# Kernel optimization log

Measured on AMD Instinct MI355X. Metric: run time of the kernel, lower is better.

The kernel has to match this reference:

```python
import jax, jax.numpy as jnp
import numpy as np

N_NODES = 50000
N_EDGES = 300000
F_IN, HID, N_CLS = 256, 256, 128


def _glorot_linear(key, fan_in, fan_out):
    # torch.nn.Linear-style uniform init, kaiming bound 1/sqrt(fan_in)
    s = 1.0 / np.sqrt(fan_in)
    return jax.random.uniform(key, (fan_in, fan_out), jnp.float32, -s, s)


def setup_inputs() -> dict:
    key = jax.random.key(0)
    ks = jax.random.split(key, 8)
    x = jax.random.normal(ks[0], (N_NODES, F_IN), jnp.float32)
    edge_index = jax.random.randint(ks[1], (2, N_EDGES), 0, N_NODES, dtype=jnp.int32)
    return {
        "x": x,
        "edge_index": edge_index,
        "W1": _glorot_linear(ks[2], F_IN, HID), "b1": jnp.zeros((HID,), jnp.float32),
        "W2": _glorot_linear(ks[3], HID, HID),  "b2": jnp.zeros((HID,), jnp.float32),
        "W3": _glorot_linear(ks[4], HID, HID),  "b3": jnp.zeros((HID,), jnp.float32),
        "W4": _glorot_linear(ks[5], HID, N_CLS), "b4": jnp.zeros((N_CLS,), jnp.float32),
    }


def _gcn_conv(x, W, b, src, dst, norm, n):
    # x' = D^{-1/2} (A + I) D^{-1/2} X W + b   (PyG GCNConv default)
    h = x @ W                                  # [N, out]
    msg = h[src] * norm[:, None]               # gather + edge scaling  [E', out]
    return jax.ops.segment_sum(msg, dst, num_segments=n) + b


def reference(x, edge_index, W1, b1, W2, b2, W3, b3, W4, b4):
    n = x.shape[0]
    loops = jnp.arange(n, dtype=edge_index.dtype)
    src = jnp.concatenate([edge_index[0], loops])  # add self-loops
    dst = jnp.concatenate([edge_index[1], loops])
    # symmetric normalization: deg over target nodes (unit edge weights)
    deg = jax.ops.segment_sum(jnp.ones_like(dst, jnp.float32), dst, num_segments=n)
    dis = jnp.where(deg > 0, jax.lax.rsqrt(jnp.maximum(deg, 1.0)), 0.0)
    norm = dis[src] * dis[dst]                     # [E']

    h = jax.nn.relu(_gcn_conv(x, W1, b1, src, dst, norm, n))
    h = jax.nn.relu(_gcn_conv(h, W2, b2, src, dst, norm, n))
    h = jax.nn.relu(_gcn_conv(h, W3, b3, src, dst, norm, n))
    h = _gcn_conv(h, W4, b4, src, dst, norm, n)    # [N, C]

    # global_add_pool with batch == zeros -> single-graph sum pool
    pooled = jnp.sum(h, axis=0, keepdims=True)     # [1, C]
    return (pooled, jax.nn.log_softmax(pooled, axis=1))
```

## Files before the change

kernel.cpp:

```cpp
#include <hip/hip_runtime.h>


typedef __attribute__((ext_vector_type(8))) short short8;
typedef __attribute__((ext_vector_type(8))) signed char schar8;
typedef __attribute__((ext_vector_type(4))) float float4v;

__device__ __forceinline__ unsigned short f2b(float f) {
    unsigned int u = __builtin_bit_cast(unsigned int, f);
    u += 0x7fffu + ((u >> 16) & 1u);
    return (unsigned short)(u >> 16);
}
__device__ __forceinline__ float b2f(unsigned short b) {
    unsigned int u = ((unsigned int)b) << 16;
    return __builtin_bit_cast(float, u);
}

__global__ void zero_convert_kernel(int* __restrict__ cnt, float* __restrict__ tsum,
                                    float* __restrict__ accbuf,
                                    const float* __restrict__ W1, const float* __restrict__ W2,
                                    const float* __restrict__ W3, unsigned short* __restrict__ Wt1,
                                    unsigned short* __restrict__ Wt2, unsigned short* __restrict__ Wt3,
                                    int N, int nb) {
    int t = threadIdx.x;
    int b = blockIdx.x;
    if (b < nb) {
        int i = b * 256 + t;
        if (i < N) { cnt[i] = 0; tsum[i] = 0.f; }
        if (b == 0) accbuf[t] = 0.f;
    } else {
        int bb = b - nb;
        int w = bb >> 8;
        int n = bb & 255;
        const float* W = (w == 0) ? W1 : (w == 1) ? W2 : W3;
        unsigned short* Wt = (w == 0) ? Wt1 : (w == 1) ? Wt2 : Wt3;
        Wt[n * 256 + t] = f2b(W[t * 256 + n]);
    }
}

__global__ void count_kernel(const int* __restrict__ dst, int* __restrict__ cnt, int E) {
    int i = blockIdx.x * blockDim.x + threadIdx.x;
    if (i < E) atomicAdd(&cnt[dst[i]], 1);
}

__global__ void blocksum_kernel(const int* __restrict__ cnt, int* __restrict__ bsum, int N) {
    __shared__ int s[256];
    int t = threadIdx.x;
    int i = blockIdx.x * 256 + t;
    s[t] = (i < N) ? cnt[i] : 0;
    __syncthreads();
    for (int d = 128; d > 0; d >>= 1) {
        if (t < d) s[t] += s[t + d];
        __syncthreads();
    }
    if (t == 0) bsum[blockIdx.x] = s[0];
}

__global__ void finalize_kernel(const int* __restrict__ cnt, const int* __restrict__ bsum,
                                int* __restrict__ offs, int* __restrict__ cursor,
                                float* __restrict__ dis, int N, int E, int nb) {
    __shared__ int bs[256];
    __shared__ int s[256];
    int t = threadIdx.x;
    bs[t] = (t < nb) ? bsum[t] : 0;
    __syncthreads();
    for (int d = 1; d < 256; d <<= 1) {
        int x = (t >= d) ? bs[t - d] : 0;
        __syncthreads();
        bs[t] += x;
        __syncthreads();
    }
    int blockoff = (blockIdx.x == 0) ? 0 : bs[blockIdx.x - 1];
    int i = blockIdx.x * 256 + t;
    int c = (i < N) ? cnt[i] : 0;
    s[t] = c;
    __syncthreads();
    for (int d = 1; d < 256; d <<= 1) {
        int x = (t >= d) ? s[t - d] : 0;
        __syncthreads();
        s[t] += x;
        __syncthreads();
    }
    if (i < N) {
        int ex = blockoff + s[t] - c;
        offs[i] = ex;
        cursor[i] = ex;
        dis[i] = rsqrtf((float)(c + 1));
    }
    if (blockIdx.x == 0 && t == 0) offs[N] = E;
}

__global__ void scatter_outsum_kernel(const int* __restrict__ src, const int* __restrict__ dst,
                                      const float* __restrict__ dis, int* __restrict__ cursor,
                                      int* __restrict__ csr_src, float* __restrict__ csr_nrm,
                                      float* __restrict__ tsum, int E) {
    int i = blockIdx.x * blockDim.x + threadIdx.x;
    if (i < E) {
        int s = src[i], d = dst[i];
        float dd = dis[d];
        int pos = atomicAdd(&cursor[d], 1);
        csr_src[pos] = s;
        csr_nrm[pos] = dis[s] * dd;
        atomicAdd(&tsum[s], dd);
    }
}

template <int AFP32>
__global__ __launch_bounds__(256, 3) void gemm_bf16_kernel(
        const void* __restrict__ Ap, const unsigned short* __restrict__ Wt,
        signed char* __restrict__ C8, float* __restrict__ Ts, int M) {
    __shared__ unsigned short As[128 * 64];
    __shared__ unsigned short Bs[128 * 64];
    const int tid = threadIdx.x;
    const int lane = tid & 63;
    const int wave = tid >> 6;
    const int l15 = lane & 15;
    const int quad = lane >> 4;
    const int wm = wave & 1;
    const int wn = wave >> 1;
    const int m0 = blockIdx.x * 128;
    const int n0 = blockIdx.y * 128;

    float4v acc[4][4] = {};

    const int lrow = lane >> 3;
    const int lslot = (lane & 7) ^ lrow;

    const unsigned short* Bt = Wt + (size_t)n0 * 256;

    for (int kk = 0; kk < 256; kk += 64) {
        if (AFP32) {
            const float* Af = (const float*)Ap;
            const int srow = tid >> 3;
            const int slot = tid & 7;
#pragma unroll
            for (int p = 0; p < 4; p++) {
                int row = p * 32 + srow;
                int gm = m0 + row;
                float4 lo = make_float4(0.f, 0.f, 0.f, 0.f);
                float4 hi = make_float4(0.f, 0.f, 0.f, 0.f);
                if (gm < M) {
                    const float* ap = &Af[(size_t)gm * 256 + kk + slot * 8];
                    lo = *(const float4*)ap;
                    hi = *(const float4*)(ap + 4);
                }
                union { unsigned short u[8]; float4 v; } pk;
                pk.u[0] = f2b(lo.x); pk.u[1] = f2b(lo.y);
                pk.u[2] = f2b(lo.z); pk.u[3] = f2b(lo.w);
                pk.u[4] = f2b(hi.x); pk.u[5] = f2b(hi.y);
                pk.u[6] = f2b(hi.z); pk.u[7] = f2b(hi.w);
                *(float4*)&As[row * 64 + 8 * (slot ^ (row & 7))] = pk.v;
            }
        } else {
            const unsigned short* Ab = (const unsigned short*)Ap;
#pragma unroll
            for (int i = 0; i < 4; i++) {
                int r0 = wave * 32 + i * 8;
                int gm = m0 + r0 + lrow;
                if (gm >= M) gm = M - 1;
                const unsigned short* gp = &Ab[(size_t)gm * 256 + kk + lslot * 8];
                __builtin_amdgcn_global_load_lds(
                    (const __attribute__((address_space(1))) unsigned int*)gp,
                    (__attribute__((address_space(3))) unsigned int*)&As[r0 * 64],
                    16, 0, 0);
            }
        }
#pragma unroll
        for (int i = 0; i < 4; i++) {
            int r0 = wave * 32 + i * 8;
            const unsigned short* gp = &Bt[(size_t)(r0 + lrow) * 256 + kk + lslot * 8];
            __builtin_amdgcn_global_load_lds(
                (const __attribute__((address_space(1))) unsigned int*)gp,
                (__attribute__((address_space(3))) unsigned int*)&Bs[r0 * 64],
                16, 0, 0);
        }
        __syncthreads();
#pragma unroll
        for (int ks = 0; ks < 64; ks += 32) {
            const int sl = (ks >> 3) + quad;
            short8 af[4], bf[4];
#pragma unroll
            for (int mi = 0; mi < 4; mi++) {
                int row = wm * 64 + mi * 16 + l15;
                af[mi] = *(const short8*)&As[row * 64 + 8 * (sl ^ (row & 7))];
            }
#pragma unroll
            for (int nj = 0; nj < 4; nj++) {
                int row = wn * 64 + nj * 16 + l15;
                bf[nj] = *(const short8*)&Bs[row * 64 + 8 * (sl ^ (row & 7))];
            }
#pragma unroll
            for (int mi = 0; mi < 4; mi++)
#pragma unroll
                for (int nj = 0; nj < 4; nj++)
                    acc[mi][nj] = __builtin_amdgcn_mfma_f32_16x16x32_bf16(
                        af[mi], bf[nj], acc[mi][nj], 0, 0, 0);
        }
        __syncthreads();
    }

    float* pmax = (float*)As;
    float* pinv = (float*)Bs;
#pragma unroll
    for (int mi = 0; mi < 4; mi++) {
#pragma unroll
        for (int r = 0; r < 4; r++) {
            float m = fabsf(acc[mi][0][r]);
            m = fmaxf(m, fabsf(acc[mi][1][r]));
            m = fmaxf(m, fabsf(acc[mi][2][r]));
            m = fmaxf(m, fabsf(acc[mi][3][r]));
            m = fmaxf(m, __shfl_xor(m, 1));
            m = fmaxf(m, __shfl_xor(m, 2));
            m = fmaxf(m, __shfl_xor(m, 4));
            m = fmaxf(m, __shfl_xor(m, 8));
            if (l15 == 0) pmax[(wm * 64 + mi * 16 + quad * 4 + r) * 2 + wn] = m;
        }
    }
    __syncthreads();
    if (tid < 128) {
        float m = fmaxf(pmax[tid * 2], pmax[tid * 2 + 1]);
        int grow = m0 + tid;
        if (grow < M) Ts[(size_t)grow * 2 + blockIdx.y] = m * (1.f / 127.f);
        pinv[tid] = (m > 0.f) ? 127.f / m : 0.f;
    }
    __syncthreads();
#pragma unroll
    for (int mi = 0; mi < 4; mi++) {
#pragma unroll
        for (int r = 0; r < 4; r++) {
            int lr = wm * 64 + mi * 16 + quad * 4 + r;
            float inv = pinv[lr];
            int row = m0 + lr;
            if (row < M) {
#pragma unroll
                for (int nj = 0; nj < 4; nj++) {
                    int col = n0 + wn * 64 + nj * 16 + l15;
                    C8[(size_t)row * 256 + col] =
                        (signed char)__float2int_rn(acc[mi][nj][r] * inv);
                }
            }
        }
    }
}

template <int RELU>
__global__ __launch_bounds__(256) void agg_bf16_kernel(
        const signed char* __restrict__ T8, const float* __restrict__ Ts,
        const float* __restrict__ bias,
        const int* __restrict__ offs, const int* __restrict__ csr_src,
        const float* __restrict__ csr_nrm, const float* __restrict__ dis,
        unsigned short* __restrict__ out, int N) {
    int hw = threadIdx.x >> 5;
    int l = threadIdx.x & 31;
    int v = blockIdx.x * 8 + hw;
    if (v >= N) return;
    int f8 = l * 8;
    int hh = l >> 4;
    int beg = offs[v], end = offs[v + 1];
    float dv = dis[v];
    float w = dv * dv * Ts[(size_t)v * 2 + hh];
    float a[8];
    {
        schar8 q = *(const schar8*)&T8[(size_t)v * 256 + f8];
#pragma unroll
        for (int i = 0; i < 8; i++) a[i] = w * (float)q[i];
    }
    int e = beg;
    for (; e + 4 <= end; e += 4) {
        int s0 = csr_src[e],     s1 = csr_src[e + 1];
        int s2 = csr_src[e + 2], s3 = csr_src[e + 3];
        float n0 = csr_nrm[e]     * Ts[(size_t)s0 * 2 + hh];
        float n1 = csr_nrm[e + 1] * Ts[(size_t)s1 * 2 + hh];
        float n2 = csr_nrm[e + 2] * Ts[(size_t)s2 * 2 + hh];
        float n3 = csr_nrm[e + 3] * Ts[(size_t)s3 * 2 + hh];
        schar8 h0 = *(const schar8*)&T8[(size_t)s0 * 256 + f8];
        schar8 h1 = *(const schar8*)&T8[(size_t)s1 * 256 + f8];
        schar8 h2 = *(const schar8*)&T8[(size_t)s2 * 256 + f8];
        schar8 h3 = *(const schar8*)&T8[(size_t)s3 * 256 + f8];
#pragma unroll
        for (int i = 0; i < 8; i++)
            a[i] += n0 * (float)h0[i] + n1 * (float)h1[i]
                  + n2 * (float)h2[i] + n3 * (float)h3[i];
    }
    for (; e < end; e++) {
        int s = csr_src[e];
        float nm = csr_nrm[e] * Ts[(size_t)s * 2 + hh];
        schar8 h = *(const schar8*)&T8[(size_t)s * 256 + f8];
#pragma unroll
        for (int i = 0; i < 8; i++) a[i] += nm * (float)h[i];
    }
    float4 bv0 = *(const float4*)&bias[f8];
    float4 bv1 = *(const float4*)&bias[f8 + 4];
    a[0] += bv0.x; a[1] += bv0.y; a[2] += bv0.z; a[3] += bv0.w;
    a[4] += bv1.x; a[5] += bv1.y; a[6] += bv1.z; a[7] += bv1.w;
    if (RELU) {
#pragma unroll
        for (int i = 0; i < 8; i++) a[i] = fmaxf(a[i], 0.f);
    }
    uint4 o;
    o.x = (unsigned int)f2b(a[0]) | ((unsigned int)f2b(a[1]) << 16);
    o.y = (unsigned int)f2b(a[2]) | ((unsigned int)f2b(a[3]) << 16);
    o.z = (unsigned int)f2b(a[4]) | ((unsigned int)f2b(a[5]) << 16);
    o.w = (unsigned int)f2b(a[6]) | ((unsigned int)f2b(a[7]) << 16);
    *(uint4*)&out[(size_t)v * 256 + f8] = o;
}

__global__ __launch_bounds__(256) void wpool_partial(
        const unsigned short* __restrict__ H, const float* __restrict__ dis,
        const float* __restrict__ tsum, float* __restrict__ partial, int N) {
    int tid = threadIdx.x;
    int f8 = (tid & 31) * 8;
    int rg = tid >> 5;
    float a[8] = {};
    for (int r = blockIdx.x * 8 + rg; r < N; r += gridDim.x * 8) {
        float s = dis[r] * (dis[r] + tsum[r]);
        short8 h = *(const short8*)&H[(size_t)r * 256 + f8];
#pragma unroll
        for (int i = 0; i < 8; i++) a[i] += s * b2f((unsigned short)h[i]);
    }
    __shared__ float red[8 * 256];
#pragma unroll
    for (int i = 0; i < 8; i++) red[rg * 256 + f8 + i] = a[i];
    __syncthreads();
    for (int s = 4; s > 0; s >>= 1) {
        if (rg < s) {
#pragma unroll
            for (int i = 0; i < 8; i++)
                red[rg * 256 + f8 + i] += red[(rg + s) * 256 + f8 + i];
        }
        __syncthreads();
    }
    partial[(size_t)blockIdx.x * 256 + tid] = red[tid];
}

__global__ void wpool_reduce(const float* __restrict__ partial, float* __restrict__ acc) {
    int f = threadIdx.x;
    int p0 = blockIdx.x * 32;
    float a = 0.f;
#pragma unroll
    for (int p = 0; p < 32; p++) a += partial[(size_t)(p0 + p) * 256 + f];
    atomicAdd(&acc[f], a);
}

__global__ void final_kernel(const float* __restrict__ acc, const float* __restrict__ W4,
                             const float* __restrict__ b4, float* __restrict__ out, int N) {
    __shared__ float red[128];
    int c = threadIdx.x;
    float p = (float)N * b4[c];
    for (int k = 0; k < 256; k++) p += acc[k] * W4[k * 128 + c];
    out[c] = p;
    red[c] = p;
    __syncthreads();
    for (int s = 64; s > 0; s >>= 1) {
        if (c < s) red[c] = fmaxf(red[c], red[c + s]);
        __syncthreads();
    }
    float m = red[0];
    __syncthreads();
    red[c] = expf(p - m);
    __syncthreads();
    for (int s = 64; s > 0; s >>= 1) {
        if (c < s) red[c] += red[c + s];
        __syncthreads();
    }
    float lse = m + logf(red[0]);
    out[128 + c] = p - lse;
}

extern "C" void kernel_launch(void* const* d_in, const int* in_sizes, int n_in,
                              void* d_out, int out_size, void* d_ws, size_t ws_size,
                              hipStream_t stream) {
    const float* x  = (const float*)d_in[0];
    const int*   ei = (const int*)d_in[1];
    const float* W1 = (const float*)d_in[2];
    const float* b1 = (const float*)d_in[3];
    const float* W2 = (const float*)d_in[4];
    const float* b2 = (const float*)d_in[5];
    const float* W3 = (const float*)d_in[6];
    const float* b3 = (const float*)d_in[7];
    const float* W4 = (const float*)d_in[8];
    const float* b4 = (const float*)d_in[9];

    const int N = in_sizes[0] / 256;
    const int E = in_sizes[1] / 2;
    const int* src = ei;
    const int* dst = ei + E;

    char* p = (char*)d_ws;
    auto alloc = [&](size_t bytes) {
        char* r = p;
        p += (bytes + 255) & ~(size_t)255;
        return r;
    };
    int*            cnt     = (int*)alloc((size_t)N * 4);
    int*            offs    = (int*)alloc((size_t)(N + 1) * 4);
    int*            cursor  = (int*)alloc((size_t)N * 4);
    float*          dis     = (float*)alloc((size_t)N * 4);
    float*          tsum    = (float*)alloc((size_t)N * 4);
    int*            bsum    = (int*)alloc(1024 * 4);
    int*            csr_src = (int*)alloc((size_t)E * 4);
    float*          csr_nrm = (float*)alloc((size_t)E * 4);
    unsigned short* Wt1     = (unsigned short*)alloc(256 * 256 * 2);
    unsigned short* Wt2     = (unsigned short*)alloc(256 * 256 * 2);
    unsigned short* Wt3     = (unsigned short*)alloc(256 * 256 * 2);
    signed char*    T8      = (signed char*)alloc((size_t)N * 256);
    float*          Ts      = (float*)alloc((size_t)N * 2 * 4);
    unsigned short* Abuf    = (unsigned short*)alloc((size_t)N * 256 * 2);
    float*          partial = (float*)alloc((size_t)1024 * 256 * 4);
    float*          accbuf  = (float*)alloc(256 * 4);

    int eb = (E + 255) / 256;
    int nb = (N + 255) / 256;
    zero_convert_kernel<<<nb + 768, 256, 0, stream>>>(cnt, tsum, accbuf,
                                                      W1, W2, W3, Wt1, Wt2, Wt3, N, nb);
    count_kernel<<<eb, 256, 0, stream>>>(dst, cnt, E);
    blocksum_kernel<<<nb, 256, 0, stream>>>(cnt, bsum, N);
    finalize_kernel<<<nb, 256, 0, stream>>>(cnt, bsum, offs, cursor, dis, N, E, nb);
    scatter_outsum_kernel<<<eb, 256, 0, stream>>>(src, dst, dis, cursor, csr_src,
                                                  csr_nrm, tsum, E);

    dim3 ggrid((N + 127) / 128, 2);
    int ab = (N + 7) / 8;
    gemm_bf16_kernel<1><<<ggrid, 256, 0, stream>>>(x, Wt1, T8, Ts, N);
    agg_bf16_kernel<1><<<ab, 256, 0, stream>>>(T8, Ts, b1, offs, csr_src, csr_nrm, dis, Abuf, N);
    gemm_bf16_kernel<0><<<ggrid, 256, 0, stream>>>(Abuf, Wt2, T8, Ts, N);
    agg_bf16_kernel<1><<<ab, 256, 0, stream>>>(T8, Ts, b2, offs, csr_src, csr_nrm, dis, Abuf, N);
    gemm_bf16_kernel<0><<<ggrid, 256, 0, stream>>>(Abuf, Wt3, T8, Ts, N);
    agg_bf16_kernel<1><<<ab, 256, 0, stream>>>(T8, Ts, b3, offs, csr_src, csr_nrm, dis, Abuf, N);

    wpool_partial<<<1024, 256, 0, stream>>>(Abuf, dis, tsum, partial, N);
    wpool_reduce<<<32, 256, 0, stream>>>(partial, accbuf);
    final_kernel<<<1, 128, 0, stream>>>(accbuf, W4, b4, (float*)d_out, N);
}
```

Measured before the change: 314.1 us.

## Double-buffer GEMM LDS tiles, pre-convert x to bf16, and swizzle block order

The GEMM now uses two LDS buffers so the async global-to-LDS load of the next K slice overlaps the MFMA work on the current one. The fp32 input x is converted to bf16 once inside the setup kernel, so the first GEMM can use the same direct-to-LDS load path as the later layers. A 1D grid with grouped block ordering puts both N-halves of neighbouring M tiles close together for better L2 reuse of A rows. In exchange, LDS use doubles and occupancy drops to 2 blocks per CU, and an extra 25MB bf16 copy of x is written and read.

```diff
diff --git a/kernel.cpp b/kernel.cpp
--- a/kernel.cpp
+++ b/kernel.cpp
@@ -20,6 +20,7 @@
                                     const float* __restrict__ W1, const float* __restrict__ W2,
                                     const float* __restrict__ W3, unsigned short* __restrict__ Wt1,
                                     unsigned short* __restrict__ Wt2, unsigned short* __restrict__ Wt3,
+                                    const float* __restrict__ x, unsigned short* __restrict__ xb,
                                     int N, int nb) {
     int t = threadIdx.x;
     int b = blockIdx.x;
@@ -27,13 +28,25 @@
         int i = b * 256 + t;
         if (i < N) { cnt[i] = 0; tsum[i] = 0.f; }
         if (b == 0) accbuf[t] = 0.f;
-    } else {
+    } else if (b < nb + 768) {
         int bb = b - nb;
         int w = bb >> 8;
         int n = bb & 255;
         const float* W = (w == 0) ? W1 : (w == 1) ? W2 : W3;
         unsigned short* Wt = (w == 0) ? Wt1 : (w == 1) ? Wt2 : Wt3;
         Wt[n * 256 + t] = f2b(W[t * 256 + n]);
+    } else {
+        size_t base = ((size_t)(b - nb - 768) * 256 + t) * 8;
+        if (base < (size_t)N * 256) {
+            float4 lo = *(const float4*)&x[base];
+            float4 hi = *(const float4*)&x[base + 4];
+            uint4 o;
+            o.x = (unsigned int)f2b(lo.x) | ((unsigned int)f2b(lo.y) << 16);
+            o.y = (unsigned int)f2b(lo.z) | ((unsigned int)f2b(lo.w) << 16);
+            o.z = (unsigned int)f2b(hi.x) | ((unsigned int)f2b(hi.y) << 16);
+            o.w = (unsigned int)f2b(hi.z) | ((unsigned int)f2b(hi.w) << 16);
+            *(uint4*)&xb[base] = o;
+        }
     }
 }
 
@@ -104,12 +117,11 @@
     }
 }
 
-template <int AFP32>
-__global__ __launch_bounds__(256, 3) void gemm_bf16_kernel(
-        const void* __restrict__ Ap, const unsigned short* __restrict__ Wt,
+__global__ __launch_bounds__(256, 2) void gemm_bf16_kernel(
+        const unsigned short* __restrict__ Ab, const unsigned short* __restrict__ Wt,
         signed char* __restrict__ C8, float* __restrict__ Ts, int M) {
-    __shared__ unsigned short As[128 * 64];
-    __shared__ unsigned short Bs[128 * 64];
+    __shared__ unsigned short As[2 * 128 * 64];
+    __shared__ unsigned short Bs[2 * 128 * 64];
     const int tid = threadIdx.x;
     const int lane = tid & 63;
     const int wave = tid >> 6;
@@ -117,8 +129,15 @@
     const int quad = lane >> 4;
     const int wm = wave & 1;
     const int wn = wave >> 1;
-    const int m0 = blockIdx.x * 128;
-    const int n0 = blockIdx.y * 128;
+
+    const int bid = blockIdx.x;
+    const int grp = bid >> 4;
+    const int ii = bid & 15;
+    const int xv = grp * 8 + (ii & 7);
+    const int yv = ii >> 3;
+    const int m0 = xv * 128;
+    const int n0 = yv * 128;
+    if (m0 >= M) return;
 
     float4v acc[4][4] = {};
 
@@ -127,53 +146,37 @@
 
     const unsigned short* Bt = Wt + (size_t)n0 * 256;
 
-    for (int kk = 0; kk < 256; kk += 64) {
-        if (AFP32) {
-            const float* Af = (const float*)Ap;
-            const int srow = tid >> 3;
-            const int slot = tid & 7;
-#pragma unroll
-            for (int p = 0; p < 4; p++) {
-                int row = p * 32 + srow;
-                int gm = m0 + row;
-                float4 lo = make_float4(0.f, 0.f, 0.f, 0.f);
-                float4 hi = make_float4(0.f, 0.f, 0.f, 0.f);
-                if (gm < M) {
-                    const float* ap = &Af[(size_t)gm * 256 + kk + slot * 8];
-                    lo = *(const float4*)ap;
-                    hi = *(const float4*)(ap + 4);
-                }
-                union { unsigned short u[8]; float4 v; } pk;
-                pk.u[0] = f2b(lo.x); pk.u[1] = f2b(lo.y);
-                pk.u[2] = f2b(lo.z); pk.u[3] = f2b(lo.w);
-                pk.u[4] = f2b(hi.x); pk.u[5] = f2b(hi.y);
-                pk.u[6] = f2b(hi.z); pk.u[7] = f2b(hi.w);
-                *(float4*)&As[row * 64 + 8 * (slot ^ (row & 7))] = pk.v;
-            }
-        } else {
-            const unsigned short* Ab = (const unsigned short*)Ap;
-#pragma unroll
-            for (int i = 0; i < 4; i++) {
-                int r0 = wave * 32 + i * 8;
-                int gm = m0 + r0 + lrow;
-                if (gm >= M) gm = M - 1;
-                const unsigned short* gp = &Ab[(size_t)gm * 256 + kk + lslot * 8];
-                __builtin_amdgcn_global_load_lds(
-                    (const __attribute__((address_space(1))) unsigned int*)gp,
-                    (__attribute__((address_space(3))) unsigned int*)&As[r0 * 64],
-                    16, 0, 0);
-            }
-        }
-#pragma unroll
-        for (int i = 0; i < 4; i++) {
-            int r0 = wave * 32 + i * 8;
-            const unsigned short* gp = &Bt[(size_t)(r0 + lrow) * 256 + kk + lslot * 8];
-            __builtin_amdgcn_global_load_lds(
-                (const __attribute__((address_space(1))) unsigned int*)gp,
-                (__attribute__((address_space(3))) unsigned int*)&Bs[r0 * 64],
-                16, 0, 0);
-        }
-        __syncthreads();
+#define GSTAGE(bufofs, kk)                                                          \
+    {                                                                               \
+        _Pragma("unroll") for (int i_ = 0; i_ < 4; i_++) {                          \
+            int r0 = wave * 32 + i_ * 8;                                            \
+            int gm = m0 + r0 + lrow;                                                \
+            if (gm >= M) gm = M - 1;                                                \
+            const unsigned short* gp = &Ab[(size_t)gm * 256 + (kk) + lslot * 8];    \
+            __builtin_amdgcn_global_load_lds(                                       \
+                (const __attribute__((address_space(1))) unsigned int*)gp,          \
+                (__attribute__((address_space(3))) unsigned int*)&As[(bufofs) + r0 * 64], \
+                16, 0, 0);                                                          \
+        }                                                                           \
+        _Pragma("unroll") for (int i_ = 0; i_ < 4; i_++) {                          \
+            int r0 = wave * 32 + i_ * 8;                                            \
+            const unsigned short* gp = &Bt[(size_t)(r0 + lrow) * 256 + (kk) + lslot * 8]; \
+            __builtin_amdgcn_global_load_lds(                                       \
+                (const __attribute__((address_space(1))) unsigned int*)gp,          \
+                (__attribute__((address_space(3))) unsigned int*)&Bs[(bufofs) + r0 * 64], \
+                16, 0, 0);                                                          \
+        }                                                                           \
+    }
+
+    GSTAGE(0, 0);
+    __syncthreads();
+    int cur = 0;
+#pragma unroll
+    for (int s = 0; s < 4; ++s) {
+        if (s < 3) GSTAGE((cur ^ 1) * 8192, (s + 1) * 64);
+        __builtin_amdgcn_sched_barrier(0);
+        const unsigned short* Ac = &As[cur * 8192];
+        const unsigned short* Bc = &Bs[cur * 8192];
 #pragma unroll
         for (int ks = 0; ks < 64; ks += 32) {
             const int sl = (ks >> 3) + quad;
@@ -181,12 +184,12 @@
 #pragma unroll
             for (int mi = 0; mi < 4; mi++) {
                 int row = wm * 64 + mi * 16 + l15;
-                af[mi] = *(const short8*)&As[row * 64 + 8 * (sl ^ (row & 7))];
+                af[mi] = *(const short8*)&Ac[row * 64 + 8 * (sl ^ (row & 7))];
             }
 #pragma unroll
             for (int nj = 0; nj < 4; nj++) {
                 int row = wn * 64 + nj * 16 + l15;
-                bf[nj] = *(const short8*)&Bs[row * 64 + 8 * (sl ^ (row & 7))];
+                bf[nj] = *(const short8*)&Bc[row * 64 + 8 * (sl ^ (row & 7))];
             }
 #pragma unroll
             for (int mi = 0; mi < 4; mi++)
@@ -196,7 +199,9 @@
                         af[mi], bf[nj], acc[mi][nj], 0, 0, 0);
         }
         __syncthreads();
-    }
+        cur ^= 1;
+    }
+#undef GSTAGE
 
     float* pmax = (float*)As;
     float* pinv = (float*)Bs;
@@ -219,7 +224,7 @@
     if (tid < 128) {
         float m = fmaxf(pmax[tid * 2], pmax[tid * 2 + 1]);
         int grow = m0 + tid;
-        if (grow < M) Ts[(size_t)grow * 2 + blockIdx.y] = m * (1.f / 127.f);
+        if (grow < M) Ts[(size_t)grow * 2 + yv] = m * (1.f / 127.f);
         pinv[tid] = (m > 0.f) ? 127.f / m : 0.f;
     }
     __syncthreads();
@@ -402,6 +407,7 @@
     unsigned short* Wt1     = (unsigned short*)alloc(256 * 256 * 2);
     unsigned short* Wt2     = (unsigned short*)alloc(256 * 256 * 2);
     unsigned short* Wt3     = (unsigned short*)alloc(256 * 256 * 2);
+    unsigned short* xb      = (unsigned short*)alloc((size_t)N * 256 * 2);
     signed char*    T8      = (signed char*)alloc((size_t)N * 256);
     float*          Ts      = (float*)alloc((size_t)N * 2 * 4);
     unsigned short* Abuf    = (unsigned short*)alloc((size_t)N * 256 * 2);
@@ -410,21 +416,23 @@
 
     int eb = (E + 255) / 256;
     int nb = (N + 255) / 256;
-    zero_convert_kernel<<<nb + 768, 256, 0, stream>>>(cnt, tsum, accbuf,
-                                                      W1, W2, W3, Wt1, Wt2, Wt3, N, nb);
+    int ncvt = (N * 32 + 255) / 256;
+    zero_convert_kernel<<<nb + 768 + ncvt, 256, 0, stream>>>(
+        cnt, tsum, accbuf, W1, W2, W3, Wt1, Wt2, Wt3, x, xb, N, nb);
     count_kernel<<<eb, 256, 0, stream>>>(dst, cnt, E);
     blocksum_kernel<<<nb, 256, 0, stream>>>(cnt, bsum, N);
     finalize_kernel<<<nb, 256, 0, stream>>>(cnt, bsum, offs, cursor, dis, N, E, nb);
     scatter_outsum_kernel<<<eb, 256, 0, stream>>>(src, dst, dis, cursor, csr_src,
                                                   csr_nrm, tsum, E);
 
-    dim3 ggrid((N + 127) / 128, 2);
+    int mtiles = (N + 127) / 128;
+    int ggrid = ((mtiles + 7) / 8) * 16;
     int ab = (N + 7) / 8;
-    gemm_bf16_kernel<1><<<ggrid, 256, 0, stream>>>(x, Wt1, T8, Ts, N);
+    gemm_bf16_kernel<<<ggrid, 256, 0, stream>>>(xb, Wt1, T8, Ts, N);
     agg_bf16_kernel<1><<<ab, 256, 0, stream>>>(T8, Ts, b1, offs, csr_src, csr_nrm, dis, Abuf, N);
-    gemm_bf16_kernel<0><<<ggrid, 256, 0, stream>>>(Abuf, Wt2, T8, Ts, N);
+    gemm_bf16_kernel<<<ggrid, 256, 0, stream>>>(Abuf, Wt2, T8, Ts, N);
     agg_bf16_kernel<1><<<ab, 256, 0, stream>>>(T8, Ts, b2, offs, csr_src, csr_nrm, dis, Abuf, N);
-    gemm_bf16_kernel<0><<<ggrid, 256, 0, stream>>>(Abuf, Wt3, T8, Ts, N);
+    gemm_bf16_kernel<<<ggrid, 256, 0, stream>>>(Abuf, Wt3, T8, Ts, N);
     agg_bf16_kernel<1><<<ab, 256, 0, stream>>>(T8, Ts, b3, offs, csr_src, csr_nrm, dis, Abuf, N);
 
     wpool_partial<<<1024, 256, 0, stream>>>(Abuf, dis, tsum, partial, N);
```

New measurement: 306.6 us. 2.4% less time.
